# Kernel tuning notes

Hardware: AMD Instinct MI355X
Metric: run time of the kernel (lower is better)

Reference implementation:

```python
import jax, jax.numpy as jnp
import numpy as np
from jax import lax

N_HEADS = 12
HEAD_DIM = 64
ALPHA = 4.0  # spikingjelly surrogate.Sigmoid default alpha
EPS = 1e-5   # BatchNorm1d default eps

@jax.custom_vjp
def _heaviside(v):
    return (v >= 0.0).astype(v.dtype)

def _heaviside_fwd(v):
    return _heaviside(v), v

def _heaviside_bwd(v, g):
    sg = jax.nn.sigmoid(ALPHA * v)
    return (g * ALPHA * sg * (1.0 - sg),)

_heaviside.defvjp(_heaviside_fwd, _heaviside_bwd)

def if_node(x):
    """Multi-step IFNode (v_threshold=1, hard reset to 0), scan over leading T dim."""
    def step(v, xt):
        v = v + xt                      # integrate
        s = _heaviside(v - 1.0)         # fire
        v = (1.0 - s) * v               # hard reset: spiked neurons -> 0
        return v, s
    _, spikes = lax.scan(step, jnp.zeros_like(x[0]), x)
    return spikes

def bn1d(x):
    """Fresh (training-mode) BatchNorm1d over (T, S, D) with channels=S;
    affine weight=1, bias=0 at init, so pure normalization over axes (0,2)."""
    mean = x.mean(axis=(0, 2), keepdims=True)
    var = x.var(axis=(0, 2), keepdims=True)  # biased variance, as torch BN uses
    return (x - mean) * lax.rsqrt(var + EPS)

def setup_inputs() -> dict:
    key = jax.random.key(0)
    ks = jax.random.split(key, 5)
    T, S, D = 4, 2048, 768
    x = jax.random.normal(ks[0], (T, S, D), dtype=jnp.float32)
    scale = 0.02
    wq = jax.random.normal(ks[1], (D, D), dtype=jnp.float32) * scale
    wk = jax.random.normal(ks[2], (D, D), dtype=jnp.float32) * scale
    wv = jax.random.normal(ks[3], (D, D), dtype=jnp.float32) * scale
    wo = jax.random.normal(ks[4], (D, D), dtype=jnp.float32) * scale
    return {"x": x, "wq": wq, "wk": wk, "wv": wv, "wo": wo, "cur_pos": S}

def reference(x, wq, wk, wv, wo, cur_pos):
    T, S, D = x.shape
    tmp = if_node(x)                    # init_spike
    Q = tmp @ wq
    V = tmp @ wv
    K = tmp @ wk
    Q = if_node(bn1d(Q))                # spike_q(bnq(Q))
    V = if_node(bn1d(V))                # spike_v(bnv(V))
    K = if_node(bn1d(K))                # spike_k(bnk(K))
    # (T, S, H, hd) -> (T, H, S, hd)
    Qh = Q.reshape(T, S, N_HEADS, HEAD_DIM).transpose(0, 2, 1, 3)
    Vh = V.reshape(T, S, N_HEADS, HEAD_DIM).transpose(0, 2, 1, 3)
    Kh = K.reshape(T, S, N_HEADS, HEAD_DIM).transpose(0, 2, 1, 3)
    QK = (Qh * Kh).sum(axis=2, keepdims=True)   # (T, H, 1, hd)
    QK = if_node(QK)                    # talking_heads
    QKV = Vh * QK                       # (T, H, S, hd)
    QKV = QKV.transpose(0, 2, 1, 3).reshape(T, S, D)
    return bn1d(QKV @ wo)
```

## Files before the change

kernel.cpp:

```cpp
#include <hip/hip_runtime.h>

#define T_ 4
#define S_ 2048
#define D_ 768
#define SD_ (S_ * D_)
#define TSD_ (T_ * SD_)
#define H_ 12
#define HD_ 64
#define PLANE_BYTES 2359296u

typedef int int32x4 __attribute__((ext_vector_type(4)));

__device__ __forceinline__ void cp16(unsigned char* lds, const unsigned char* g) {
    __builtin_amdgcn_global_load_lds(
        (const __attribute__((address_space(1))) unsigned int*)g,
        (__attribute__((address_space(3))) unsigned int*)lds, 16, 0, 0);
}

__global__ __launch_bounds__(256) void k_prep_w(const float* __restrict__ wq,
                                                const float* __restrict__ wk,
                                                const float* __restrict__ wv,
                                                const float* __restrict__ wo,
                                                unsigned char* __restrict__ Bp) {
    const float* W = (blockIdx.y == 0) ? wq : (blockIdx.y == 1) ? wk
                   : (blockIdx.y == 2) ? wv : wo;
    unsigned char* out = Bp + (size_t)blockIdx.y * PLANE_BYTES;
    int idx = blockIdx.x * 256 + threadIdx.x;
    int j0 = idx & 3;
    int lane = (idx >> 2) & 63;
    int kb = (idx >> 8) % 12;
    int rest = (idx >> 8) / 12;
    int nbg = rest % 48;
    int p = rest / 48;
    int n = nbg * 16 + (lane & 15);
    int kbase = kb * 64 + (lane >> 4) * 16 + j0 * 4;
    unsigned int packed = 0;
#pragma unroll
    for (int jj = 0; jj < 4; jj++) {
        float w = W[(size_t)(kbase + jj) * D_ + n];
        int u = (int)rintf(w * 1073741824.0f);
        for (int i = 0; i < p; i++) u = (u + 128) >> 8;
        packed |= ((unsigned int)(u & 255)) << (8 * jj);
    }
    *(unsigned int*)(out + (size_t)idx * 4) = packed;
}

__global__ __launch_bounds__(256) void k_ifnode_x(const float* __restrict__ x,
                                                  unsigned char* __restrict__ As) {
    int i = blockIdx.x * blockDim.x + threadIdx.x;
    int idx = i * 4;
    if (idx >= SD_) return;
    double v[4] = {0.0, 0.0, 0.0, 0.0};
#pragma unroll
    for (int t = 0; t < T_; t++) {
        float4 xt = *(const float4*)(x + (size_t)t * SD_ + idx);
        float xs[4] = {xt.x, xt.y, xt.z, xt.w};
        uchar4 sp;
        unsigned char* so = &sp.x;
#pragma unroll
        for (int j = 0; j < 4; j++) {
            v[j] += (double)xs[j];
            unsigned char s = (v[j] >= 1.0) ? 1 : 0;
            so[j] = s;
            if (s) v[j] = 0.0;
        }
        *(uchar4*)(As + (size_t)t * SD_ + idx) = sp;
    }
}

#define LDSBUF 24576

__global__ __launch_bounds__(256, 2) void k_gemm_i8(
    const unsigned char* __restrict__ A,
    const unsigned char* __restrict__ Bp,
    const unsigned char* __restrict__ Ms,
    float* __restrict__ C0, float* __restrict__ C1, float* __restrict__ C2,
    int bzoff) {
    int z = blockIdx.z;
    const unsigned char* B = Bp + (size_t)(bzoff + z) * PLANE_BYTES;
    float* C = (z == 0) ? C0 : (z == 1) ? C1 : C2;

    __shared__ __align__(16) unsigned char smem[2 * LDSBUF];

    int tid = threadIdx.x;
    int lane = tid & 63;
    int w = tid >> 6;
    int wm = w >> 1;
    int wn = w & 1;
    int row0 = blockIdx.x * 128;
    int tI = row0 >> 11;
    int n0 = blockIdx.y * 64;
    int nbg0 = blockIdx.y * 4;
    int col = lane & 15;
    int quad = lane >> 4;

    int32x4 zerov = {0, 0, 0, 0};
    int32x4 acc[4][2][4];
#pragma unroll
    for (int mb = 0; mb < 4; mb++)
#pragma unroll
        for (int nb = 0; nb < 2; nb++)
#pragma unroll
            for (int p = 0; p < 4; p++) acc[mb][nb][p] = zerov;

    const unsigned char* gA0 = A + (size_t)(row0 + (2 * w) * 16 + (lane >> 2)) * D_
                                 + (lane & 3) * 16;
    const unsigned char* gA1 = gA0 + (size_t)16 * D_;

    auto stage = [&](int buf, int kb) {
        unsigned char* ab = smem + buf * LDSBUF;
        cp16(ab + (2 * w + 0) * 1024, gA0 + kb * 64);
        cp16(ab + (2 * w + 1) * 1024, gA1 + kb * 64);
        unsigned char* bb = ab + 8192;
#pragma unroll
        for (int qi = 0; qi < 4; qi++) {
            int q = 4 * w + qi;
            int p = q >> 2, nb = q & 3;
            const unsigned char* gB =
                B + ((size_t)((p * 48 + nbg0 + nb) * 12 + kb) * 64 + lane) * 16;
            cp16(bb + q * 1024, gB);
        }
    };

    stage(0, 0);
    __syncthreads();

    for (int kb = 0; kb < 12; kb++) {
        int cur = kb & 1;
        if (kb < 11) stage(1 - cur, kb + 1);
        const unsigned char* ab = smem + cur * LDSBUF;
        int32x4 af[4];
#pragma unroll
        for (int mb = 0; mb < 4; mb++)
            af[mb] = *(const int32x4*)(
                ab + (wm * 64 + mb * 16 + col) * 64 + quad * 16);
        if (Ms) {
            int32x4 mv = *(const int32x4*)(Ms + tI * D_ + kb * 64 + quad * 16);
#pragma unroll
            for (int mb = 0; mb < 4; mb++) af[mb] &= mv;
        }
        const unsigned char* bb = ab + 8192;
#pragma unroll
        for (int p = 0; p < 4; p++)
#pragma unroll
            for (int nb = 0; nb < 2; nb++) {
                int32x4 bf = *(const int32x4*)(
                    bb + ((p * 4 + wn * 2 + nb) * 64 + lane) * 16);
#pragma unroll
                for (int mb = 0; mb < 4; mb++)
                    acc[mb][nb][p] = __builtin_amdgcn_mfma_i32_16x16x64_i8(
                        af[mb], bf, acc[mb][nb][p], 0, 0, 0);
            }
        __syncthreads();
    }

#pragma unroll
    for (int mb = 0; mb < 4; mb++)
#pragma unroll
        for (int nb = 0; nb < 2; nb++)
#pragma unroll
            for (int r = 0; r < 4; r++) {
                long t = (long)acc[mb][nb][0][r] + ((long)acc[mb][nb][1][r] << 8)
                       + ((long)acc[mb][nb][2][r] << 16)
                       + ((long)acc[mb][nb][3][r] << 24);
                float v = (float)((double)t * (1.0 / 1073741824.0));
                int rr = row0 + wm * 64 + mb * 16 + quad * 4 + r;
                int cc = n0 + wn * 32 + nb * 16 + col;
                C[(size_t)rr * D_ + cc] = v;
            }
}

__global__ __launch_bounds__(256) void k_bn_if(const float* __restrict__ Qf,
                                               const float* __restrict__ Kf,
                                               const float* __restrict__ Vf,
                                               unsigned char* __restrict__ Qs,
                                               unsigned char* __restrict__ Ks,
                                               unsigned char* __restrict__ Vs) {
    int s = blockIdx.x;
    int y = blockIdx.y;
    const float* X = (y == 0) ? Qf : (y == 1) ? Kf : Vf;
    unsigned char* Sp = (y == 0) ? Qs : (y == 1) ? Ks : Vs;

    __shared__ float buf[T_][D_];
    __shared__ double red[16];

    int tid = threadIdx.x;
    double sum = 0.0, sumsq = 0.0;
#pragma unroll
    for (int t = 0; t < T_; t++) {
        for (int d = tid; d < D_; d += 256) {
            float v = X[(size_t)t * SD_ + (size_t)s * D_ + d];
            buf[t][d] = v;
            double dv = (double)v;
            sum += dv;
            sumsq += dv * dv;
        }
    }
#pragma unroll
    for (int off = 32; off > 0; off >>= 1) {
        sum += __shfl_down(sum, off);
        sumsq += __shfl_down(sumsq, off);
    }
    int lane = tid & 63, wv = tid >> 6;
    if (lane == 0) { red[wv] = sum; red[4 + wv] = sumsq; }
    __syncthreads();
    if (tid == 0) {
        double s4 = red[0] + red[1] + red[2] + red[3];
        double q4 = red[4] + red[5] + red[6] + red[7];
        double mean = s4 / 3072.0;
        double var = q4 / 3072.0 - mean * mean;
        red[8] = mean;
        red[9] = 1.0 / sqrt(var + 1e-5);
    }
    __syncthreads();
    double mean = red[8], rstd = red[9];
    for (int d = tid; d < D_; d += 256) {
        double v = 0.0;
#pragma unroll
        for (int t = 0; t < T_; t++) {
            double xn = ((double)buf[t][d] - mean) * rstd;
            v += xn;
            int sp = (v >= 1.0) ? 1 : 0;
            Sp[(size_t)t * SD_ + (size_t)s * D_ + d] = (unsigned char)sp;
            if (sp) v = 0.0;
        }
    }
}

__global__ __launch_bounds__(256) void k_qk(const unsigned char* __restrict__ Qs,
                                            const unsigned char* __restrict__ Ks,
                                            float* __restrict__ QK) {
    int b = blockIdx.x;
    int ch = b & 15;
    int th = b >> 4;
    int t = th / H_;
    int h = th % H_;
    int dq = threadIdx.x & 15;
    int sl = threadIdx.x >> 4;
    const unsigned int* qb = (const unsigned int*)(Qs + (size_t)t * SD_ + h * HD_);
    const unsigned int* kb = (const unsigned int*)(Ks + (size_t)t * SD_ + h * HD_);
    int s0 = ch * 128;
    unsigned int acc = 0;
    for (int s = s0 + sl; s < s0 + 128; s += 16)
        acc += (qb[s * 192 + dq] & kb[s * 192 + dq]);
    __shared__ unsigned int part[16][16];
    part[sl][dq] = acc;
    __syncthreads();
    if (sl == 0) {
        unsigned int tot = 0;
#pragma unroll
        for (int i = 0; i < 16; i++) tot += part[i][dq];
#pragma unroll
        for (int j = 0; j < 4; j++) {
            float v = (float)((tot >> (8 * j)) & 255u);
            atomicAdd(&QK[t * D_ + h * HD_ + dq * 4 + j], v);
        }
    }
}

__global__ __launch_bounds__(256) void k_if_qk(const float* __restrict__ QK,
                                               unsigned char* __restrict__ QKm) {
    int j = blockIdx.x * 256 + threadIdx.x;
    if (j >= D_) return;
    float v = 0.f;
#pragma unroll
    for (int t = 0; t < T_; t++) {
        v += QK[t * D_ + j];
        unsigned char sp = (v >= 1.0f) ? 1 : 0;
        QKm[t * D_ + j] = sp;
        if (sp) v = 0.f;
    }
}

__global__ __launch_bounds__(256) void k_bn_out(const float* __restrict__ Xin,
                                                float* __restrict__ out) {
    int s = blockIdx.x;
    __shared__ float buf[T_][D_];
    __shared__ double red[16];
    int tid = threadIdx.x;
    double sum = 0.0, sumsq = 0.0;
#pragma unroll
    for (int t = 0; t < T_; t++) {
        for (int d = tid; d < D_; d += 256) {
            float v = Xin[(size_t)t * SD_ + (size_t)s * D_ + d];
            buf[t][d] = v;
            double dv = (double)v;
            sum += dv;
            sumsq += dv * dv;
        }
    }
#pragma unroll
    for (int off = 32; off > 0; off >>= 1) {
        sum += __shfl_down(sum, off);
        sumsq += __shfl_down(sumsq, off);
    }
    int lane = tid & 63, wv = tid >> 6;
    if (lane == 0) { red[wv] = sum; red[4 + wv] = sumsq; }
    __syncthreads();
    if (tid == 0) {
        double s4 = red[0] + red[1] + red[2] + red[3];
        double q4 = red[4] + red[5] + red[6] + red[7];
        double mean = s4 / 3072.0;
        double var = q4 / 3072.0 - mean * mean;
        red[8] = mean;
        red[9] = 1.0 / sqrt(var + 1e-5);
    }
    __syncthreads();
    double mean = red[8], rstd = red[9];
    for (int d = tid; d < D_; d += 256) {
#pragma unroll
        for (int t = 0; t < T_; t++) {
            double v = (double)buf[t][d];
            out[(size_t)t * SD_ + (size_t)s * D_ + d] =
                (float)((v - mean) * rstd);
        }
    }
}

extern "C" void kernel_launch(void* const* d_in, const int* in_sizes, int n_in,
                              void* d_out, int out_size, void* d_ws,
                              size_t ws_size, hipStream_t stream) {
    const float* x  = (const float*)d_in[0];
    const float* wq = (const float*)d_in[1];
    const float* wk = (const float*)d_in[2];
    const float* wv = (const float*)d_in[3];
    const float* wo = (const float*)d_in[4];
    float* out = (float*)d_out;

    float* ws  = (float*)d_ws;
    float* Qf  = ws;
    float* Kf  = ws + (size_t)TSD_;
    float* Vf  = ws + (size_t)2 * TSD_;
    float* QK  = ws + (size_t)3 * TSD_;
    unsigned char* QKm = (unsigned char*)(QK + T_ * D_);
    unsigned char* Sx  = QKm + 4096;
    unsigned char* Ks  = Sx + (size_t)TSD_;
    unsigned char* Vs  = Ks + (size_t)TSD_;
    unsigned char* Bp  = Vs + (size_t)TSD_;
    unsigned char* Qs  = Sx;

    hipMemsetAsync(QK, 0, T_ * D_ * sizeof(float), stream);
    k_prep_w<<<dim3(589824 / 256, 4), 256, 0, stream>>>(wq, wk, wv, wo, Bp);
    k_ifnode_x<<<SD_ / (4 * 256), 256, 0, stream>>>(x, Sx);
    k_gemm_i8<<<dim3(64, 12, 3), 256, 0, stream>>>(Sx, Bp, nullptr,
                                                   Qf, Kf, Vf, 0);
    k_bn_if<<<dim3(S_, 3), 256, 0, stream>>>(Qf, Kf, Vf, Qs, Ks, Vs);
    k_qk<<<T_ * H_ * 16, 256, 0, stream>>>(Qs, Ks, QK);
    k_if_qk<<<3, 256, 0, stream>>>(QK, QKm);
    k_gemm_i8<<<dim3(64, 12, 1), 256, 0, stream>>>(Vs, Bp, QKm, Qf, Qf, Qf, 3);
    k_bn_out<<<S_, 256, 0, stream>>>(Qf, out);
}
```

Measured before the change: 228.0 us.

## Store spike activations in MFMA fragment layout and load A directly to registers

Spike tensors (Sx, Q/K/V spikes) are now written in a pre-tiled MFMA fragment layout, so the GEMM reads A fragments straight from global memory into registers with prefetch instead of staging them through LDS. The GEMM tile shrinks from 128 to 64 rows, with a smaller LDS buffer and occupancy hint 3, and the grid doubles. Weight prep and the x IF-node kernel are fused into one launch. The QK reduction is rewritten to use the new layout with one block per (t,h) and no atomics or memset. The trade-off is scattered byte writes in the bn_if kernel and less reuse of B per block.

```diff
diff --git a/kernel.cpp b/kernel.cpp
--- a/kernel.cpp
+++ b/kernel.cpp
@@ -17,60 +17,68 @@
         (__attribute__((address_space(3))) unsigned int*)lds, 16, 0, 0);
 }
 
-__global__ __launch_bounds__(256) void k_prep_w(const float* __restrict__ wq,
-                                                const float* __restrict__ wk,
-                                                const float* __restrict__ wv,
-                                                const float* __restrict__ wo,
-                                                unsigned char* __restrict__ Bp) {
-    const float* W = (blockIdx.y == 0) ? wq : (blockIdx.y == 1) ? wk
-                   : (blockIdx.y == 2) ? wv : wo;
-    unsigned char* out = Bp + (size_t)blockIdx.y * PLANE_BYTES;
-    int idx = blockIdx.x * 256 + threadIdx.x;
-    int j0 = idx & 3;
-    int lane = (idx >> 2) & 63;
-    int kb = (idx >> 8) % 12;
-    int rest = (idx >> 8) / 12;
-    int nbg = rest % 48;
-    int p = rest / 48;
-    int n = nbg * 16 + (lane & 15);
-    int kbase = kb * 64 + (lane >> 4) * 16 + j0 * 4;
-    unsigned int packed = 0;
-#pragma unroll
-    for (int jj = 0; jj < 4; jj++) {
-        float w = W[(size_t)(kbase + jj) * D_ + n];
-        int u = (int)rintf(w * 1073741824.0f);
-        for (int i = 0; i < p; i++) u = (u + 128) >> 8;
-        packed |= ((unsigned int)(u & 255)) << (8 * jj);
-    }
-    *(unsigned int*)(out + (size_t)idx * 4) = packed;
-}
-
-__global__ __launch_bounds__(256) void k_ifnode_x(const float* __restrict__ x,
-                                                  unsigned char* __restrict__ As) {
-    int i = blockIdx.x * blockDim.x + threadIdx.x;
-    int idx = i * 4;
-    if (idx >= SD_) return;
-    double v[4] = {0.0, 0.0, 0.0, 0.0};
-#pragma unroll
-    for (int t = 0; t < T_; t++) {
-        float4 xt = *(const float4*)(x + (size_t)t * SD_ + idx);
-        float xs[4] = {xt.x, xt.y, xt.z, xt.w};
-        uchar4 sp;
-        unsigned char* so = &sp.x;
-#pragma unroll
-        for (int j = 0; j < 4; j++) {
-            v[j] += (double)xs[j];
-            unsigned char s = (v[j] >= 1.0) ? 1 : 0;
-            so[j] = s;
-            if (s) v[j] = 0.0;
-        }
-        *(uchar4*)(As + (size_t)t * SD_ + idx) = sp;
-    }
-}
-
-#define LDSBUF 24576
-
-__global__ __launch_bounds__(256, 2) void k_gemm_i8(
+__device__ __forceinline__ size_t frag_addr(int m, int d) {
+    return ((size_t)(m >> 4) * 12 + (d >> 6)) * 1024 +
+           (size_t)(((d >> 4) & 3) * 256 + (m & 15) * 16 + (d & 15));
+}
+
+__global__ __launch_bounds__(256) void k_prep_all(const float* __restrict__ wq,
+                                                  const float* __restrict__ wk,
+                                                  const float* __restrict__ wv,
+                                                  const float* __restrict__ wo,
+                                                  const float* __restrict__ x,
+                                                  unsigned char* __restrict__ Bp,
+                                                  unsigned char* __restrict__ Sx) {
+    if (blockIdx.y < 4) {
+        const float* W = (blockIdx.y == 0) ? wq : (blockIdx.y == 1) ? wk
+                       : (blockIdx.y == 2) ? wv : wo;
+        unsigned char* out = Bp + (size_t)blockIdx.y * PLANE_BYTES;
+        int idx = blockIdx.x * 256 + threadIdx.x;
+        int j0 = idx & 3;
+        int lane = (idx >> 2) & 63;
+        int kb = (idx >> 8) % 12;
+        int rest = (idx >> 8) / 12;
+        int nbg = rest % 48;
+        int p = rest / 48;
+        int n = nbg * 16 + (lane & 15);
+        int kbase = kb * 64 + (lane >> 4) * 16 + j0 * 4;
+        unsigned int packed = 0;
+#pragma unroll
+        for (int jj = 0; jj < 4; jj++) {
+            float w = W[(size_t)(kbase + jj) * D_ + n];
+            int u = (int)rintf(w * 1073741824.0f);
+            for (int i = 0; i < p; i++) u = (u + 128) >> 8;
+            packed |= ((unsigned int)(u & 255)) << (8 * jj);
+        }
+        *(unsigned int*)(out + (size_t)idx * 4) = packed;
+    } else {
+        int i = blockIdx.x * 256 + threadIdx.x;
+        int idx = i * 4;
+        if (idx >= SD_) return;
+        int s = idx / D_;
+        int d = idx % D_;
+        double v[4] = {0.0, 0.0, 0.0, 0.0};
+#pragma unroll
+        for (int t = 0; t < T_; t++) {
+            float4 xt = *(const float4*)(x + (size_t)t * SD_ + idx);
+            float xs[4] = {xt.x, xt.y, xt.z, xt.w};
+            uchar4 sp;
+            unsigned char* so = &sp.x;
+#pragma unroll
+            for (int j = 0; j < 4; j++) {
+                v[j] += (double)xs[j];
+                unsigned char ss = (v[j] >= 1.0) ? 1 : 0;
+                so[j] = ss;
+                if (ss) v[j] = 0.0;
+            }
+            *(uchar4*)(Sx + frag_addr(t * S_ + s, d)) = sp;
+        }
+    }
+}
+
+#define LDSBUF 16384
+
+__global__ __launch_bounds__(256, 3) void k_gemm_i8(
     const unsigned char* __restrict__ A,
     const unsigned char* __restrict__ Bp,
     const unsigned char* __restrict__ Ms,
@@ -87,7 +95,7 @@
     int w = tid >> 6;
     int wm = w >> 1;
     int wn = w & 1;
-    int row0 = blockIdx.x * 128;
+    int row0 = blockIdx.x * 64;
     int tI = row0 >> 11;
     int n0 = blockIdx.y * 64;
     int nbg0 = blockIdx.y * 4;
@@ -95,67 +103,66 @@
     int quad = lane >> 4;
 
     int32x4 zerov = {0, 0, 0, 0};
-    int32x4 acc[4][2][4];
-#pragma unroll
-    for (int mb = 0; mb < 4; mb++)
+    int32x4 acc[2][2][4];
+#pragma unroll
+    for (int mb = 0; mb < 2; mb++)
 #pragma unroll
         for (int nb = 0; nb < 2; nb++)
 #pragma unroll
             for (int p = 0; p < 4; p++) acc[mb][nb][p] = zerov;
 
-    const unsigned char* gA0 = A + (size_t)(row0 + (2 * w) * 16 + (lane >> 2)) * D_
-                                 + (lane & 3) * 16;
-    const unsigned char* gA1 = gA0 + (size_t)16 * D_;
+    const unsigned char* Abase =
+        A + ((size_t)((row0 >> 4) + wm * 2) * 12) * 1024 + lane * 16;
 
     auto stage = [&](int buf, int kb) {
-        unsigned char* ab = smem + buf * LDSBUF;
-        cp16(ab + (2 * w + 0) * 1024, gA0 + kb * 64);
-        cp16(ab + (2 * w + 1) * 1024, gA1 + kb * 64);
-        unsigned char* bb = ab + 8192;
+        unsigned char* bb = smem + buf * LDSBUF;
 #pragma unroll
         for (int qi = 0; qi < 4; qi++) {
             int q = 4 * w + qi;
             int p = q >> 2, nb = q & 3;
-            const unsigned char* gB =
-                B + ((size_t)((p * 48 + nbg0 + nb) * 12 + kb) * 64 + lane) * 16;
-            cp16(bb + q * 1024, gB);
+            cp16(bb + q * 1024,
+                 B + (size_t)((p * 48 + nbg0 + nb) * 12 + kb) * 1024 + lane * 16);
         }
     };
 
+    int32x4 a_cur[2], a_nxt[2];
+    a_cur[0] = *(const int32x4*)(Abase);
+    a_cur[1] = *(const int32x4*)(Abase + 12288);
     stage(0, 0);
     __syncthreads();
 
     for (int kb = 0; kb < 12; kb++) {
         int cur = kb & 1;
-        if (kb < 11) stage(1 - cur, kb + 1);
-        const unsigned char* ab = smem + cur * LDSBUF;
-        int32x4 af[4];
-#pragma unroll
-        for (int mb = 0; mb < 4; mb++)
-            af[mb] = *(const int32x4*)(
-                ab + (wm * 64 + mb * 16 + col) * 64 + quad * 16);
+        if (kb < 11) {
+            stage(1 - cur, kb + 1);
+            a_nxt[0] = *(const int32x4*)(Abase + (kb + 1) * 1024);
+            a_nxt[1] = *(const int32x4*)(Abase + 12288 + (kb + 1) * 1024);
+        }
+        int32x4 af0 = a_cur[0], af1 = a_cur[1];
         if (Ms) {
             int32x4 mv = *(const int32x4*)(Ms + tI * D_ + kb * 64 + quad * 16);
-#pragma unroll
-            for (int mb = 0; mb < 4; mb++) af[mb] &= mv;
-        }
-        const unsigned char* bb = ab + 8192;
+            af0 &= mv;
+            af1 &= mv;
+        }
+        const unsigned char* bb = smem + cur * LDSBUF;
 #pragma unroll
         for (int p = 0; p < 4; p++)
 #pragma unroll
             for (int nb = 0; nb < 2; nb++) {
                 int32x4 bf = *(const int32x4*)(
-                    bb + ((p * 4 + wn * 2 + nb) * 64 + lane) * 16);
-#pragma unroll
-                for (int mb = 0; mb < 4; mb++)
-                    acc[mb][nb][p] = __builtin_amdgcn_mfma_i32_16x16x64_i8(
-                        af[mb], bf, acc[mb][nb][p], 0, 0, 0);
+                    bb + (size_t)(p * 4 + wn * 2 + nb) * 1024 + lane * 16);
+                acc[0][nb][p] = __builtin_amdgcn_mfma_i32_16x16x64_i8(
+                    af0, bf, acc[0][nb][p], 0, 0, 0);
+                acc[1][nb][p] = __builtin_amdgcn_mfma_i32_16x16x64_i8(
+                    af1, bf, acc[1][nb][p], 0, 0, 0);
             }
         __syncthreads();
-    }
-
-#pragma unroll
-    for (int mb = 0; mb < 4; mb++)
+        a_cur[0] = a_nxt[0];
+        a_cur[1] = a_nxt[1];
+    }
+
+#pragma unroll
+    for (int mb = 0; mb < 2; mb++)
 #pragma unroll
         for (int nb = 0; nb < 2; nb++)
 #pragma unroll
@@ -164,7 +171,7 @@
                        + ((long)acc[mb][nb][2][r] << 16)
                        + ((long)acc[mb][nb][3][r] << 24);
                 float v = (float)((double)t * (1.0 / 1073741824.0));
-                int rr = row0 + wm * 64 + mb * 16 + quad * 4 + r;
+                int rr = row0 + wm * 32 + mb * 16 + quad * 4 + r;
                 int cc = n0 + wn * 32 + nb * 16 + col;
                 C[(size_t)rr * D_ + cc] = v;
             }
@@ -221,7 +228,7 @@
             double xn = ((double)buf[t][d] - mean) * rstd;
             v += xn;
             int sp = (v >= 1.0) ? 1 : 0;
-            Sp[(size_t)t * SD_ + (size_t)s * D_ + d] = (unsigned char)sp;
+            Sp[frag_addr(t * S_ + s, d)] = (unsigned char)sp;
             if (sp) v = 0.0;
         }
     }
@@ -230,31 +237,37 @@
 __global__ __launch_bounds__(256) void k_qk(const unsigned char* __restrict__ Qs,
                                             const unsigned char* __restrict__ Ks,
                                             float* __restrict__ QK) {
-    int b = blockIdx.x;
-    int ch = b & 15;
-    int th = b >> 4;
-    int t = th / H_;
-    int h = th % H_;
-    int dq = threadIdx.x & 15;
-    int sl = threadIdx.x >> 4;
-    const unsigned int* qb = (const unsigned int*)(Qs + (size_t)t * SD_ + h * HD_);
-    const unsigned int* kb = (const unsigned int*)(Ks + (size_t)t * SD_ + h * HD_);
-    int s0 = ch * 128;
-    unsigned int acc = 0;
-    for (int s = s0 + sl; s < s0 + 128; s += 16)
-        acc += (qb[s * 192 + dq] & kb[s * 192 + dq]);
-    __shared__ unsigned int part[16][16];
-    part[sl][dq] = acc;
-    __syncthreads();
-    if (sl == 0) {
+    int t = blockIdx.x / H_;
+    int h = blockIdx.x % H_;
+    int lane = threadIdx.x & 63;
+    int w = threadIdx.x >> 6;
+    size_t base = ((size_t)t * 128 * 12 + h) * 1024 + lane * 16;
+    uint4 acc = make_uint4(0, 0, 0, 0);
+    for (int c = w; c < 128; c += 4) {
+        uint4 q = *(const uint4*)(Qs + base + (size_t)c * 12288);
+        uint4 k = *(const uint4*)(Ks + base + (size_t)c * 12288);
+        acc.x += q.x & k.x;
+        acc.y += q.y & k.y;
+        acc.z += q.z & k.z;
+        acc.w += q.w & k.w;
+    }
+    __shared__ unsigned int part[4][64][4];
+    part[w][lane][0] = acc.x;
+    part[w][lane][1] = acc.y;
+    part[w][lane][2] = acc.z;
+    part[w][lane][3] = acc.w;
+    __syncthreads();
+    if (threadIdx.x < 64) {
+        int quad = threadIdx.x >> 4;
+        int rem = threadIdx.x & 15;
+        int dw = rem >> 2;
+        int b = rem & 3;
         unsigned int tot = 0;
 #pragma unroll
-        for (int i = 0; i < 16; i++) tot += part[i][dq];
-#pragma unroll
-        for (int j = 0; j < 4; j++) {
-            float v = (float)((tot >> (8 * j)) & 255u);
-            atomicAdd(&QK[t * D_ + h * HD_ + dq * 4 + j], v);
-        }
+        for (int ww = 0; ww < 4; ww++)
+            for (int cc = 0; cc < 16; cc++)
+                tot += (part[ww][quad * 16 + cc][dw] >> (8 * b)) & 255u;
+        QK[t * D_ + h * HD_ + quad * 16 + dw * 4 + b] = (float)tot;
     }
 }
 
@@ -339,14 +352,13 @@
     unsigned char* Bp  = Vs + (size_t)TSD_;
     unsigned char* Qs  = Sx;
 
-    hipMemsetAsync(QK, 0, T_ * D_ * sizeof(float), stream);
-    k_prep_w<<<dim3(589824 / 256, 4), 256, 0, stream>>>(wq, wk, wv, wo, Bp);
-    k_ifnode_x<<<SD_ / (4 * 256), 256, 0, stream>>>(x, Sx);
-    k_gemm_i8<<<dim3(64, 12, 3), 256, 0, stream>>>(Sx, Bp, nullptr,
-                                                   Qf, Kf, Vf, 0);
+    k_prep_all<<<dim3(589824 / 256, 5), 256, 0, stream>>>(wq, wk, wv, wo, x,
+                                                          Bp, Sx);
+    k_gemm_i8<<<dim3(128, 12, 3), 256, 0, stream>>>(Sx, Bp, nullptr,
+                                                    Qf, Kf, Vf, 0);
     k_bn_if<<<dim3(S_, 3), 256, 0, stream>>>(Qf, Kf, Vf, Qs, Ks, Vs);
-    k_qk<<<T_ * H_ * 16, 256, 0, stream>>>(Qs, Ks, QK);
+    k_qk<<<T_ * H_, 256, 0, stream>>>(Qs, Ks, QK);
     k_if_qk<<<3, 256, 0, stream>>>(QK, QKm);
-    k_gemm_i8<<<dim3(64, 12, 1), 256, 0, stream>>>(Vs, Bp, QKm, Qf, Qf, Qf, 3);
+    k_gemm_i8<<<dim3(128, 12, 1), 256, 0, stream>>>(Vs, Bp, QKm, Qf, Qf, Qf, 3);
     k_bn_out<<<S_, 256, 0, stream>>>(Qf, out);
 }
```

After: 239.1 us. 1.05x slower.
